# Performance work log

Measured on AMD Instinct MI355X. Metric: run time of the kernel, lower is better.

The kernel has to match this reference:

```python
import jax, jax.numpy as jnp
import numpy as np

# Production-scale dims (see shape_source)
L, H, W = 8, 1536, 1536            # layers, grid height, grid width
C = 12                              # number of inter-layer connections
MAX_DIST, TAU = 5, 2.0              # LocalConnectivity distance kernel
DECAY, THRESH, BETA = 0.9, 0.0, 10.0  # SpikeNode params (decay_rate, spike_threshold, surrogate_beta)

# fixed connection topology (src_layer -> dst_layer), mirrors init connections list
_PAIRS = [(0,1),(1,2),(2,3),(3,4),(4,5),(5,6),(6,7),(0,2),(2,4),(4,6),(7,0),(3,5)]


def _distance_kernel():
    ks = 2 * MAX_DIST + 1
    yy, xx = np.meshgrid(np.arange(ks) - MAX_DIST, np.arange(ks) - MAX_DIST, indexing='ij')
    dist = np.sqrt(yy.astype(np.float64) ** 2 + xx.astype(np.float64) ** 2)
    kern = np.exp(-dist / TAU)
    kern[dist > MAX_DIST] = 0.0
    kern[MAX_DIST, MAX_DIST] = 0.0  # no self-connection
    return jnp.asarray(kern, jnp.float32)


def setup_inputs() -> dict:
    key = jax.random.key(0)
    k1, k2, k3, k4, k5 = jax.random.split(key, 5)
    external = jax.random.normal(k1, (L, H, W), jnp.float32)
    prev_spikes = (jax.random.uniform(k2, (L, H, W)) < 0.1).astype(jnp.float32)
    membrane = jax.random.normal(k3, (L, H, W), jnp.float32) * 0.5
    refractory = jax.random.randint(k4, (L, H, W), 0, 4).astype(jnp.int32)
    inter_weights = jax.random.normal(k5, (C, H, W), jnp.float32) * 0.1
    conn_src = jnp.asarray([p[0] for p in _PAIRS], jnp.int32)
    conn_dst = jnp.asarray([p[1] for p in _PAIRS], jnp.int32)
    return {
        'external': external,
        'prev_spikes': prev_spikes,
        'membrane': membrane,
        'inter_weights': inter_weights,
        'local_kernel': _distance_kernel(),
        'refractory': refractory,
        'conn_src': conn_src,
        'conn_dst': conn_dst,
    }


def reference(external, prev_spikes, membrane, inter_weights, local_kernel,
              refractory, conn_src, conn_dst):
    # --- LocalConnectivity: distance-decay lateral conv on previous spikes ---
    # treat L as batch, single channel; SAME padding keeps [L,H,W]
    internal = jax.lax.conv_general_dilated(
        prev_spikes[:, None, :, :], local_kernel[None, None, :, :],
        window_strides=(1, 1), padding='SAME')[:, 0]

    # --- inter-layer axonal input: sum over connections into each dst layer ---
    contrib = prev_spikes[conn_src] * inter_weights          # [C,H,W]
    axonal = jax.ops.segment_sum(contrib, conn_dst, num_segments=L)  # [L,H,W]

    # --- SpikeNode single CLK step (LIF + refractory + surrogate spike) ---
    total = external + internal + axonal
    active = (refractory == 0).astype(total.dtype)           # not in refractory period
    v_new = DECAY * membrane + active * total
    surr = jax.nn.sigmoid(BETA * (v_new - THRESH))           # surrogate (for grads)
    hard = (v_new > THRESH).astype(total.dtype)              # hard Heaviside forward
    spikes = (hard + surr - jax.lax.stop_gradient(surr)) * active  # straight-through
    return spikes
```

## Files before the change

### kernel.cpp

```cpp
#include <hip/hip_runtime.h>
#include <cmath>

namespace {

constexpr int L = 8, H = 1536, W = 1536, HW = H * W, C = 12;
constexpr int TWB = 128, TH = 8;
constexpr int LH = TH + 10;
constexpr int LPAD = 8;
constexpr int LCOLS = 148;
constexpr int NSLOT = 36;
constexpr int NSTG  = LH * NSLOT;

__device__ __host__ constexpr int XLO[11]  = {5, 2, 1, 1, 1, 0, 1, 1, 1, 2, 5};
__device__ __host__ constexpr int XHI[11]  = {5, 8, 9, 9, 9,10, 9, 9, 9, 8, 5};
__device__ __host__ constexpr int WOFF[11] = {0, 1, 8,17,26,35,46,55,64,73,80};

__device__ constexpr int CSRC[C] = {0,1,2,3,4,5,6,0,2,4,7,3};
__device__ constexpr int CDST[C] = {1,2,3,4,5,6,7,2,4,6,0,5};

struct Weights { float w[81]; };

__global__ __launch_bounds__(128)
void snn_fast(const float* __restrict__ ext,
              const float* __restrict__ spk,
              const float* __restrict__ mem,
              const float* __restrict__ iw,
              const int*   __restrict__ refr,
              float* __restrict__ out,
              unsigned*    wslist,
              unsigned     cap,
              const Weights wt)
{
    __shared__ float tile[LH][LCOLS];

    const int tx = threadIdx.x;
    const int ty = threadIdx.y;
    const int tid = ty * 32 + tx;
    const int bx = blockIdx.x, by = blockIdx.y, l = blockIdx.z;

    const int gx0 = bx * TWB - LPAD;
    const int gy0 = by * TH - 5;
    const float* sp_l = spk + l * HW;
    for (int idx = tid; idx < NSTG; idx += 128) {
        const int r    = idx / NSLOT;
        const int slot = idx - r * NSLOT;
        const int gy = gy0 + r;
        const int gx = gx0 + 4 * slot;
        float4 v = make_float4(0.f, 0.f, 0.f, 0.f);
        if ((unsigned)gy < (unsigned)H) {
            const float* src = sp_l + gy * W;
            if (gx >= 0 && gx + 3 < W) {
                v = *(const float4*)(src + gx);
            } else {
                float t0 = 0.f, t1 = 0.f, t2 = 0.f, t3 = 0.f;
                if ((unsigned)(gx + 0) < (unsigned)W) t0 = src[gx + 0];
                if ((unsigned)(gx + 1) < (unsigned)W) t1 = src[gx + 1];
                if ((unsigned)(gx + 2) < (unsigned)W) t2 = src[gx + 2];
                if ((unsigned)(gx + 3) < (unsigned)W) t3 = src[gx + 3];
                v = make_float4(t0, t1, t2, t3);
            }
        }
        *(float4*)&tile[r][4 * slot] = v;
    }
    __syncthreads();

    float acc[2][4] = {{0.f,0.f,0.f,0.f},{0.f,0.f,0.f,0.f}};
    #pragma unroll
    for (int j = 0; j < 12; ++j) {
        const float* row = &tile[ty * 2 + j][0];
        alignas(16) float win[20];
        *(float4*)&win[0]  = *(const float4*)&row[4 * tx + 0];
        *(float4*)&win[4]  = *(const float4*)&row[4 * tx + 4];
        *(float4*)&win[8]  = *(const float4*)&row[4 * tx + 8];
        *(float4*)&win[12] = *(const float4*)&row[4 * tx + 12];
        win[16] = row[4 * tx + 16];
        #pragma unroll
        for (int k = 0; k < 2; ++k) {
            const int dy = j - k;
            if (dy < 0 || dy > 10) continue;
            #pragma unroll
            for (int dx = XLO[dy]; dx <= XHI[dy]; ++dx) {
                const float wv = wt.w[WOFF[dy] + dx - XLO[dy]];
                #pragma unroll
                for (int c = 0; c < 4; ++c)
                    acc[k][c] += wv * win[3 + c + dx];
            }
        }
    }

    const int ox = bx * TWB + 4 * tx;
    #pragma unroll
    for (int k = 0; k < 2; ++k) {
        const int oy   = by * TH + ty * 2 + k;
        const int pidx = oy * W + ox;
        const int gidx = l * HW + pidx;

        const int4   rf4 = *(const int4*)  (refr + gidx);
        const float4 e4  = *(const float4*)(ext  + gidx);
        const float4 m4  = *(const float4*)(mem  + gidx);

        float ax0 = 0.f, ax1 = 0.f, ax2 = 0.f, ax3 = 0.f;
        #pragma unroll
        for (int c = 0; c < C; ++c) {
            if (CDST[c] != l) continue;
            const float4 s4 = *(const float4*)(spk + CSRC[c] * HW + pidx);
            const float4 w4 = *(const float4*)(iw  + c       * HW + pidx);
            ax0 += s4.x * w4.x; ax1 += s4.y * w4.y;
            ax2 += s4.z * w4.z; ax3 += s4.w * w4.w;
        }
        const float ee[4] = {e4.x, e4.y, e4.z, e4.w};
        const float mm[4] = {m4.x, m4.y, m4.z, m4.w};
        const int   rr[4] = {rf4.x, rf4.y, rf4.z, rf4.w};
        const float aa[4] = {ax0, ax1, ax2, ax3};
        float res[4];
        #pragma unroll
        for (int c = 0; c < 4; ++c) {
            const float v = 0.9f * mm[c] + (ee[c] + acc[k][c] + aa[c]);
            res[c] = (rr[c] == 0 && v > 0.f) ? 1.f : 0.f;
            if (rr[c] == 0 && __builtin_expect(fabsf(v) < 1e-3f, 0)) {
                const unsigned idx = atomicAdd(wslist, 1u);
                if (idx < cap) wslist[1 + idx] = (unsigned)(gidx + c);
            }
        }
        *(float4*)(out + gidx) = make_float4(res[0], res[1], res[2], res[3]);
    }
}

__global__ __launch_bounds__(256)
void snn_fixup(const float* __restrict__ ext,
               const float* __restrict__ spk,
               const float* __restrict__ mem,
               const float* __restrict__ iw,
               const float* __restrict__ lk,
               float* __restrict__ out,
               const unsigned* __restrict__ wslist,
               unsigned cap)
{
    const unsigned n = min(wslist[0], cap);
    for (unsigned i = blockIdx.x * blockDim.x + threadIdx.x; i < n;
         i += gridDim.x * blockDim.x) {
        const unsigned gidx = wslist[1 + i];
        const int l    = gidx / HW;
        const int pidx = gidx - l * HW;
        const int oy   = pidx / W;
        const int ox   = pidx - oy * W;

        const float* sp = spk + l * HW;
        double conv = 0.0;
        for (int dy = 0; dy < 11; ++dy) {
            const int yy = oy + dy - 5;
            if ((unsigned)yy >= (unsigned)H) continue;
            for (int dx = 0; dx < 11; ++dx) {
                const int xx = ox + dx - 5;
                if ((unsigned)xx >= (unsigned)W) continue;
                conv += (double)lk[dy * 11 + dx] * (double)sp[yy * W + xx];
            }
        }
        double ax = 0.0;
        #pragma unroll
        for (int c = 0; c < C; ++c)
            if (CDST[c] == l)
                ax += (double)spk[CSRC[c] * HW + pidx] * (double)iw[c * HW + pidx];
        const double tot = ((double)ext[gidx] + conv) + ax;
        const double vd  = 0.9 * (double)mem[gidx] + tot;
        out[gidx] = (vd > 0.0) ? 1.f : 0.f;
    }
}

}

extern "C" void kernel_launch(void* const* d_in, const int* in_sizes, int n_in,
                              void* d_out, int out_size, void* d_ws, size_t ws_size,
                              hipStream_t stream) {
    const float* ext  = (const float*)d_in[0];
    const float* spk  = (const float*)d_in[1];
    const float* mem  = (const float*)d_in[2];
    const float* iw   = (const float*)d_in[3];
    const float* lk   = (const float*)d_in[4];
    const int*   refr = (const int*)  d_in[5];
    float* o = (float*)d_out;

    Weights wt;
    for (int dy = 0; dy < 11; ++dy) {
        for (int dx = XLO[dy]; dx <= XHI[dy]; ++dx) {
            const double ddy = dy - 5, ddx = dx - 5;
            const double dist = std::sqrt(ddy * ddy + ddx * ddx);
            double w = std::exp(-dist / 2.0);
            if (dist > 5.0) w = 0.0;
            if (dy == 5 && dx == 5) w = 0.0;
            wt.w[WOFF[dy] + dx - XLO[dy]] = (float)w;
        }
    }

    dim3 grid(W / TWB, H / TH, L);
    dim3 block(32, 4, 1);

    unsigned* wsl = (unsigned*)d_ws;
    size_t cap64 = ws_size / 4 - 1;
    const unsigned cap = (unsigned)(cap64 > 0x7FFFFFFFu ? 0x7FFFFFFFu : cap64);
    hipMemsetAsync(d_ws, 0, 4, stream);
    hipLaunchKernelGGL(snn_fast, grid, block, 0, stream,
                       ext, spk, mem, iw, refr, o, wsl, cap, wt);
    hipLaunchKernelGGL(snn_fixup, dim3(64), dim3(256), 0, stream,
                       ext, spk, mem, iw, lk, o, wsl, cap);
}
```

Baseline: 193.6 us.

## Use one output row per thread with 256-thread blocks and early global loads

Doubles the block to 32x8 threads so each thread computes one output row of four pixels instead of two rows. The global loads of ext, mem, refractory and the axonal terms are issued before the shared-memory convolution so their latency can overlap with it, and the accumulator is seeded with the membrane and external terms. This gives more threads per block and fewer registers per thread. In exchange, each thread loses the reuse of shared-memory rows across two output rows, so the number of LDS reads per output goes up.

```diff
diff --git a/kernel.cpp b/kernel.cpp
--- a/kernel.cpp
+++ b/kernel.cpp
@@ -20,7 +20,7 @@
 
 struct Weights { float w[81]; };
 
-__global__ __launch_bounds__(128)
+__global__ __launch_bounds__(256)
 void snn_fast(const float* __restrict__ ext,
               const float* __restrict__ spk,
               const float* __restrict__ mem,
@@ -41,7 +41,7 @@
     const int gx0 = bx * TWB - LPAD;
     const int gy0 = by * TH - 5;
     const float* sp_l = spk + l * HW;
-    for (int idx = tid; idx < NSTG; idx += 128) {
+    for (int idx = tid; idx < NSTG; idx += 256) {
         const int r    = idx / NSLOT;
         const int slot = idx - r * NSLOT;
         const int gy = gy0 + r;
@@ -52,72 +52,71 @@
             if (gx >= 0 && gx + 3 < W) {
                 v = *(const float4*)(src + gx);
             } else {
-                float t0 = 0.f, t1 = 0.f, t2 = 0.f, t3 = 0.f;
-                if ((unsigned)(gx + 0) < (unsigned)W) t0 = src[gx + 0];
-                if ((unsigned)(gx + 1) < (unsigned)W) t1 = src[gx + 1];
-                if ((unsigned)(gx + 2) < (unsigned)W) t2 = src[gx + 2];
-                if ((unsigned)(gx + 3) < (unsigned)W) t3 = src[gx + 3];
-                v = make_float4(t0, t1, t2, t3);
+                if ((unsigned)(gx + 0) < (unsigned)W) v.x = src[gx + 0];
+                if ((unsigned)(gx + 1) < (unsigned)W) v.y = src[gx + 1];
+                if ((unsigned)(gx + 2) < (unsigned)W) v.z = src[gx + 2];
+                if ((unsigned)(gx + 3) < (unsigned)W) v.w = src[gx + 3];
             }
         }
         *(float4*)&tile[r][4 * slot] = v;
     }
     __syncthreads();
 
-    float acc[2][4] = {{0.f,0.f,0.f,0.f},{0.f,0.f,0.f,0.f}};
-    #pragma unroll
-    for (int j = 0; j < 12; ++j) {
-        const float* row = &tile[ty * 2 + j][0];
-        alignas(16) float win[20];
-        *(float4*)&win[0]  = *(const float4*)&row[4 * tx + 0];
-        *(float4*)&win[4]  = *(const float4*)&row[4 * tx + 4];
-        *(float4*)&win[8]  = *(const float4*)&row[4 * tx + 8];
-        *(float4*)&win[12] = *(const float4*)&row[4 * tx + 12];
-        win[16] = row[4 * tx + 16];
-        #pragma unroll
-        for (int k = 0; k < 2; ++k) {
-            const int dy = j - k;
-            if (dy < 0 || dy > 10) continue;
-            #pragma unroll
-            for (int dx = XLO[dy]; dx <= XHI[dy]; ++dx) {
-                const float wv = wt.w[WOFF[dy] + dx - XLO[dy]];
-                #pragma unroll
-                for (int c = 0; c < 4; ++c)
-                    acc[k][c] += wv * win[3 + c + dx];
-            }
-        }
-    }
-
-    const int ox = bx * TWB + 4 * tx;
-    #pragma unroll
-    for (int k = 0; k < 2; ++k) {
-        const int oy   = by * TH + ty * 2 + k;
-        const int pidx = oy * W + ox;
-        const int gidx = l * HW + pidx;
-
+    const int ox   = bx * TWB + 4 * tx;
+    const int oy   = by * TH + ty;
+    const int pidx = oy * W + ox;
+    const int gidx = l * HW + pidx;
+
+    float acc[4];
+    unsigned mask = 0;
+    {
         const int4   rf4 = *(const int4*)  (refr + gidx);
         const float4 e4  = *(const float4*)(ext  + gidx);
         const float4 m4  = *(const float4*)(mem  + gidx);
-
-        float ax0 = 0.f, ax1 = 0.f, ax2 = 0.f, ax3 = 0.f;
+        acc[0] = fmaf(0.9f, m4.x, e4.x);
+        acc[1] = fmaf(0.9f, m4.y, e4.y);
+        acc[2] = fmaf(0.9f, m4.z, e4.z);
+        acc[3] = fmaf(0.9f, m4.w, e4.w);
+        mask |= (rf4.x == 0 ? 1u : 0u) << 0;
+        mask |= (rf4.y == 0 ? 1u : 0u) << 1;
+        mask |= (rf4.z == 0 ? 1u : 0u) << 2;
+        mask |= (rf4.w == 0 ? 1u : 0u) << 3;
         #pragma unroll
         for (int c = 0; c < C; ++c) {
             if (CDST[c] != l) continue;
             const float4 s4 = *(const float4*)(spk + CSRC[c] * HW + pidx);
             const float4 w4 = *(const float4*)(iw  + c       * HW + pidx);
-            ax0 += s4.x * w4.x; ax1 += s4.y * w4.y;
-            ax2 += s4.z * w4.z; ax3 += s4.w * w4.w;
-        }
-        const float ee[4] = {e4.x, e4.y, e4.z, e4.w};
-        const float mm[4] = {m4.x, m4.y, m4.z, m4.w};
-        const int   rr[4] = {rf4.x, rf4.y, rf4.z, rf4.w};
-        const float aa[4] = {ax0, ax1, ax2, ax3};
+            acc[0] += s4.x * w4.x; acc[1] += s4.y * w4.y;
+            acc[2] += s4.z * w4.z; acc[3] += s4.w * w4.w;
+        }
+    }
+
+    #pragma unroll
+    for (int dy = 0; dy < 11; ++dy) {
+        const float* row = &tile[ty + dy][4 * tx];
+        alignas(16) float win[20];
+        *(float4*)&win[0]  = *(const float4*)(row + 0);
+        *(float4*)&win[4]  = *(const float4*)(row + 4);
+        *(float4*)&win[8]  = *(const float4*)(row + 8);
+        *(float4*)&win[12] = *(const float4*)(row + 12);
+        win[16] = row[16];
+        #pragma unroll
+        for (int dx = XLO[dy]; dx <= XHI[dy]; ++dx) {
+            const float wv = wt.w[WOFF[dy] + dx - XLO[dy]];
+            #pragma unroll
+            for (int c = 0; c < 4; ++c)
+                acc[c] += wv * win[3 + c + dx];
+        }
+    }
+
+    {
         float res[4];
         #pragma unroll
         for (int c = 0; c < 4; ++c) {
-            const float v = 0.9f * mm[c] + (ee[c] + acc[k][c] + aa[c]);
-            res[c] = (rr[c] == 0 && v > 0.f) ? 1.f : 0.f;
-            if (rr[c] == 0 && __builtin_expect(fabsf(v) < 1e-3f, 0)) {
+            const bool act = (mask >> c) & 1u;
+            const float v = acc[c];
+            res[c] = (act && v > 0.f) ? 1.f : 0.f;
+            if (act && __builtin_expect(fabsf(v) < 1e-3f, 0)) {
                 const unsigned idx = atomicAdd(wslist, 1u);
                 if (idx < cap) wslist[1 + idx] = (unsigned)(gidx + c);
             }
@@ -193,7 +192,7 @@
     }
 
     dim3 grid(W / TWB, H / TH, L);
-    dim3 block(32, 4, 1);
+    dim3 block(32, 8, 1);
 
     unsigned* wsl = (unsigned*)d_ws;
     size_t cap64 = ws_size / 4 - 1;
```

Result: slower. 290.3 us (+49.9%).
